# Kernel optimization log

Hardware: AMD Instinct MI355X
Metric: run time of the kernel (lower is better)

Reference implementation:

```python
import jax, jax.numpy as jnp
import numpy as np

# irreps: node in/out = 32x0e + 16x1o (dim 80), sh = 1x0e + 1x1o (dim 4)
N_NODES, N_EDGES = 8000, 64000
NUM_BASIS, RAD_HIDDEN = 8, 64
WEIGHT_NUMEL = 2304  # 32*32 + 32*16 + 16*16 + 16*32
EPS = 1e-8
INV_SQRT3 = 1.0 / np.sqrt(3.0)
# e3nn path weights (normalization='component', path_normalization='element'):
# into 0e outputs: sqrt(ir.dim=1 / (32+16)); into 1o outputs: sqrt(3 / (32+16))
PW0 = float(np.sqrt(1.0 / 48.0))
PW1 = float(np.sqrt(3.0 / 48.0))


def setup_inputs() -> dict:
    key = jax.random.key(0)
    ks = jax.random.split(key, 10)
    node_features = jax.random.normal(ks[0], (N_NODES, 80), dtype=jnp.float32)
    edge_index = jax.random.randint(ks[1], (2, N_EDGES), 0, N_NODES, dtype=jnp.int64)
    edge_sh = jax.random.normal(ks[2], (N_EDGES, 4), dtype=jnp.float32)
    edge_radial_emb = jax.random.uniform(ks[3], (N_EDGES, NUM_BASIS), dtype=jnp.float32)
    # RadialMLP params (Linear 8->64, SiLU, Linear 64->2304)
    rW1 = jax.random.normal(ks[4], (NUM_BASIS, RAD_HIDDEN), dtype=jnp.float32) / np.sqrt(NUM_BASIS)
    rb1 = jnp.zeros((RAD_HIDDEN,), dtype=jnp.float32)
    rW2 = jax.random.normal(ks[5], (RAD_HIDDEN, WEIGHT_NUMEL), dtype=jnp.float32) / np.sqrt(RAD_HIDDEN)
    rb2 = jnp.zeros((WEIGHT_NUMEL,), dtype=jnp.float32)
    # o3.Linear weights (per-irrep mixing matrices, e3nn init ~ N(0,1))
    Wl0 = jax.random.normal(ks[6], (32, 32), dtype=jnp.float32)
    Wl1 = jax.random.normal(ks[7], (16, 16), dtype=jnp.float32)
    return {"node_features": node_features, "edge_index": edge_index,
            "edge_sh": edge_sh, "edge_radial_emb": edge_radial_emb,
            "rW1": rW1, "rb1": rb1, "rW2": rW2, "rb2": rb2,
            "Wl0": Wl0, "Wl1": Wl1}


def reference(node_features, edge_index, edge_sh, edge_radial_emb,
              rW1, rb1, rW2, rb2, Wl0, Wl1):
    N = node_features.shape[0]
    src, dst = edge_index[0], edge_index[1]
    # radial MLP -> per-edge tensor-product weights [E, 2304] (fp32 path)
    h = jax.nn.silu(edge_radial_emb @ rW1 + rb1)
    tpw = h @ rW2 + rb2
    E = tpw.shape[0]
    wA = tpw[:, :1024].reshape(E, 32, 32)      # 0e x 0e -> 0e
    wB = tpw[:, 1024:1536].reshape(E, 32, 16)  # 0e x 1o -> 1o
    wC = tpw[:, 1536:1792].reshape(E, 16, 16)  # 1o x 0e -> 1o
    wD = tpw[:, 1792:2304].reshape(E, 16, 32)  # 1o x 1o -> 0e
    # gather source node features
    xs = node_features[src, :32]                       # [E,32] scalars
    xv = node_features[src, 32:].reshape(E, 16, 3)     # [E,16,3] vectors
    sh0 = edge_sh[:, 0]                                # [E]
    shv = edge_sh[:, 1:4]                              # [E,3]
    # equivariant tensor product messages
    dotv = jnp.einsum('euk,ek->eu', xv, shv)           # 1o.1o -> 0e
    msg_s = PW0 * (jnp.einsum('euw,eu->ew', wA, xs * sh0[:, None])
                   + INV_SQRT3 * jnp.einsum('euw,eu->eu' if False else 'euw,eu->ew', wD, dotv))
    msg_v = (PW1 * INV_SQRT3) * (jnp.einsum('euw,eu,ek->ewk', wB, xs, shv)
                                 + jnp.einsum('euw,euk->ewk', wC, xv) * sh0[:, None, None])
    messages = jnp.concatenate([msg_s, msg_v.reshape(E, 48)], axis=-1)  # [E,80]
    # scatter-sum aggregation over destination nodes
    agg = jax.ops.segment_sum(messages, dst, num_segments=N)            # [N,80]
    # equivariant linear (per-irrep mixing, fan-in normalized)
    lin_s = (agg[:, :32] @ Wl0) / np.sqrt(32.0)
    lin_v = jnp.einsum('nuk,uv->nvk', agg[:, 32:].reshape(N, 16, 3), Wl1) / np.sqrt(16.0)
    # SafeNormActivation: silu on scalars, norm-gated silu on vectors
    act_s = jax.nn.silu(lin_s)
    norms = jnp.linalg.norm(lin_v, axis=-1, keepdims=True)   # [N,16,1]
    safe = jnp.maximum(norms, EPS)
    act_v = jnp.where(norms < EPS, 0.0, (lin_v / safe) * jax.nn.silu(norms))
    activated = jnp.concatenate([act_s, act_v.reshape(N, 48)], axis=-1)
    # skip connection (irreps_in == irreps_out -> identity skip)
    return node_features + activated
```

## Files before the change

### kernel.cpp

```cpp
#include <hip/hip_runtime.h>
#include <math.h>

#define N_NODES_C 8000
#define N_EDGES_C 64000

static constexpr float PW0_C     = 0.14433756729740646f;
static constexpr float C1_C      = 0.14433756729740643f;
static constexpr float PW0IS3_C  = 0.08333333333333333f;
static constexpr float RS32_C    = 0.17677669529663687f;

typedef __attribute__((ext_vector_type(8))) short short8;
typedef __attribute__((ext_vector_type(4))) float f32x4;

__device__ __forceinline__ float silu_f(float x) { return x / (1.0f + expf(-x)); }

__device__ __forceinline__ unsigned short f2bf(float x) {
    union { float f; unsigned u; } a; a.f = x;
    unsigned r = a.u + 0x7fffu + ((a.u >> 16) & 1u);
    return (unsigned short)(r >> 16);
}
__device__ __forceinline__ float bf2f(unsigned short x) {
    union { unsigned u; float f; } a; a.u = ((unsigned)x) << 16; return a.f;
}

__device__ __forceinline__ void stage16(const void* g, void* lds) {
    __builtin_amdgcn_global_load_lds(
        (const __attribute__((address_space(1))) void*)g,
        (__attribute__((address_space(3))) void*)lds, 16, 0, 0);
}

__global__ __launch_bounds__(256) void prep_kernel(
    const float* __restrict__ rW2, unsigned short* __restrict__ rW2T)
{
    const int idx = blockIdx.x * 256 + threadIdx.x;
    const int k = idx / 2304, col = idx % 2304;
    rW2T[(size_t)col * 64 + k] = f2bf(rW2[idx]);
}

__global__ __launch_bounds__(256, 2) void edge_kernel_mfma(
    const float* __restrict__ nf,
    const int*   __restrict__ ei,
    const float* __restrict__ sh,
    const float* __restrict__ emb,
    const float* __restrict__ rW1,
    const float* __restrict__ rb1,
    const unsigned short* __restrict__ rW2T,
    const float* __restrict__ rb2,
    float* __restrict__ agg)
{
    __shared__ float pool_f[8192];
    __shared__ float rb2_s[2304];
    __shared__ float rW1_s[512];
    __shared__ unsigned short xs_s[128][34];
    __shared__ unsigned short xv_s[128][50];
    __shared__ float dv_s[128][17];
    __shared__ float sh0_s[128];
    __shared__ float shv_s[128][3];
    __shared__ int   dst_s[128];

    char*  stg = (char*)pool_f;
    float (*msg)[84] = reinterpret_cast<float(*)[84]>(pool_f);

    const int t    = threadIdx.x;
    const int e0   = blockIdx.x * 128;
    const int lane = t & 63, wv = t >> 6;
    const int l15  = lane & 15, lk = lane >> 4;
    const int l7   = l15 & 7;

    #define STAGE(cc, b) {                                                        \
        const char* gsrc = (const char*)rW2T + (size_t)(cc) * 8192;               \
        _Pragma("unroll")                                                         \
        for (int j = 0; j < 2; j++) {                                             \
            const int p  = j * 256 + t;                                           \
            const int pr = p >> 3;                                                \
            const int sl = (p & 7) ^ (pr & 7);                                    \
            stage16(gsrc + pr * 128 + (sl << 4), stg + (b) * 8192 + p * 16);      \
        }                                                                         \
    }

    STAGE(0, 0)
    STAGE(1, 1)
    if (t < 128) {
        const int eid = e0 + t;
        dst_s[t] = ei[N_EDGES_C + eid];
        const float4 s4 = *reinterpret_cast<const float4*>(sh + (size_t)eid * 4);
        sh0_s[t] = s4.x;
        shv_s[t][0] = s4.y; shv_s[t][1] = s4.z; shv_s[t][2] = s4.w;
    }
    {
        const int e = t >> 1, q = t & 1;
        const int src = ei[e0 + e];
        const float* p = nf + (size_t)src * 80 + q * 40;
        #pragma unroll
        for (int f4 = 0; f4 < 10; f4++) {
            const float4 v = *reinterpret_cast<const float4*>(p + f4 * 4);
            const int g = q * 40 + f4 * 4;
            const float vv[4] = {v.x, v.y, v.z, v.w};
            #pragma unroll
            for (int ii = 0; ii < 4; ii++) {
                const int gg = g + ii;
                if (gg < 32) xs_s[e][gg]      = f2bf(vv[ii]);
                else         xv_s[e][gg - 32] = f2bf(vv[ii]);
            }
        }
    }
    for (int i = t; i < 512;  i += 256) rW1_s[i] = rW1[i];
    for (int i = t; i < 2304; i += 256) rb2_s[i] = rb2[i];
    __syncthreads();

    {
        const int e = t >> 1, u0d = (t & 1) * 8;
        #pragma unroll
        for (int i = 0; i < 8; i++) {
            const int u = u0d + i;
            dv_s[e][u] = bf2f(xv_s[e][u*3+0]) * shv_s[e][0]
                       + bf2f(xv_s[e][u*3+1]) * shv_s[e][1]
                       + bf2f(xv_s[e][u*3+2]) * shv_s[e][2];
        }
    }
    const int eA = wv * 32 + l15;
    const int eB = eA + 16;
    short8 bfr[2][2];
    {
        float embA[8], embB[8];
        {
            const float* pa = emb + (size_t)(e0 + eA) * 8;
            const float* pb = emb + (size_t)(e0 + eB) * 8;
            const float4 a0 = *reinterpret_cast<const float4*>(pa);
            const float4 a1 = *reinterpret_cast<const float4*>(pa + 4);
            const float4 b0 = *reinterpret_cast<const float4*>(pb);
            const float4 b1 = *reinterpret_cast<const float4*>(pb + 4);
            embA[0]=a0.x; embA[1]=a0.y; embA[2]=a0.z; embA[3]=a0.w;
            embA[4]=a1.x; embA[5]=a1.y; embA[6]=a1.z; embA[7]=a1.w;
            embB[0]=b0.x; embB[1]=b0.y; embB[2]=b0.z; embB[3]=b0.w;
            embB[4]=b1.x; embB[5]=b1.y; embB[6]=b1.z; embB[7]=b1.w;
        }
        #pragma unroll
        for (int s = 0; s < 2; s++) {
            const int k0 = s * 32 + lk * 8;
            const float4 r0 = *reinterpret_cast<const float4*>(rb1 + k0);
            const float4 r1 = *reinterpret_cast<const float4*>(rb1 + k0 + 4);
            float preA[8] = {r0.x,r0.y,r0.z,r0.w, r1.x,r1.y,r1.z,r1.w};
            float preB[8] = {r0.x,r0.y,r0.z,r0.w, r1.x,r1.y,r1.z,r1.w};
            #pragma unroll
            for (int b = 0; b < 8; b++) {
                const float4 wa = *reinterpret_cast<const float4*>(&rW1_s[b * 64 + k0]);
                const float4 wb = *reinterpret_cast<const float4*>(&rW1_s[b * 64 + k0 + 4]);
                const float wv4[8] = {wa.x,wa.y,wa.z,wa.w, wb.x,wb.y,wb.z,wb.w};
                #pragma unroll
                for (int j = 0; j < 8; j++) {
                    preA[j] = fmaf(embA[b], wv4[j], preA[j]);
                    preB[j] = fmaf(embB[b], wv4[j], preB[j]);
                }
            }
            short8 hA, hBv;
            #pragma unroll
            for (int j = 0; j < 8; j++) {
                hA[j]  = (short)f2bf(silu_f(preA[j]));
                hBv[j] = (short)f2bf(silu_f(preB[j]));
            }
            bfr[0][s] = hA; bfr[1][s] = hBv;
        }
    }
    const float sh0A = sh0_s[eA], sh0B = sh0_s[eB];
    const float fAA  = PW0_C * sh0A, fAB = PW0_C * sh0B;
    __syncthreads();

    float sA0[2][4] = {{0,0,0,0},{0,0,0,0}}, sA1[2][4] = {{0,0,0,0},{0,0,0,0}};
    float sB0[4] = {0,0,0,0},                sB1[4] = {0,0,0,0};
    float sC0[3][4] = {{0,0,0,0},{0,0,0,0},{0,0,0,0}};
    float sC1[3][4] = {{0,0,0,0},{0,0,0,0},{0,0,0,0}};

    for (int c = 0; c < 36; ++c) {
        if (c < 34) STAGE(c + 2, (c + 2) & 3)
        if (c < 34)       { asm volatile("s_waitcnt vmcnt(4)" ::: "memory"); }
        else if (c == 34) { asm volatile("s_waitcnt vmcnt(2)" ::: "memory"); }
        else              { asm volatile("s_waitcnt vmcnt(0)" ::: "memory"); }
        __builtin_amdgcn_sched_barrier(0);
        __builtin_amdgcn_s_barrier();

        const int cb = c * 64;
        f32x4 acc0[4], acc1[4];
        #pragma unroll
        for (int m = 0; m < 4; m++) {
            const float4 rbv = *reinterpret_cast<const float4*>(&rb2_s[cb + m * 16 + lk * 4]);
            acc0[m][0] = rbv.x; acc0[m][1] = rbv.y; acc0[m][2] = rbv.z; acc0[m][3] = rbv.w;
            acc1[m][0] = rbv.x; acc1[m][1] = rbv.y; acc1[m][2] = rbv.z; acc1[m][3] = rbv.w;
        }
        const char* sb = stg + (c & 3) * 8192;
        #pragma unroll
        for (int s = 0; s < 2; s++) {
            #pragma unroll
            for (int m = 0; m < 4; m++) {
                const short8 a = *reinterpret_cast<const short8*>(
                    sb + (m * 16 + l15) * 128 + (((s * 4 + lk) ^ l7) << 4));
                acc0[m] = __builtin_amdgcn_mfma_f32_16x16x32_bf16(a, bfr[0][s], acc0[m], 0, 0, 0);
                acc1[m] = __builtin_amdgcn_mfma_f32_16x16x32_bf16(a, bfr[1][s], acc1[m], 0, 0, 0);
            }
        }

        if (c < 16) {
            const float xA0 = bf2f(xs_s[eA][c*2]) * fAA, xA1 = bf2f(xs_s[eA][c*2+1]) * fAA;
            const float xB0 = bf2f(xs_s[eB][c*2]) * fAB, xB1 = bf2f(xs_s[eB][c*2+1]) * fAB;
            #pragma unroll
            for (int r = 0; r < 4; r++) {
                sA0[0][r] = fmaf(acc0[0][r], xA0, fmaf(acc0[2][r], xA1, sA0[0][r]));
                sA0[1][r] = fmaf(acc0[1][r], xA0, fmaf(acc0[3][r], xA1, sA0[1][r]));
                sA1[0][r] = fmaf(acc1[0][r], xB0, fmaf(acc1[2][r], xB1, sA1[0][r]));
                sA1[1][r] = fmaf(acc1[1][r], xB0, fmaf(acc1[3][r], xB1, sA1[1][r]));
            }
        } else if (c < 24) {
            const int u0 = (c - 16) * 4;
            float xA[4], xB[4];
            #pragma unroll
            for (int m = 0; m < 4; m++) { xA[m] = bf2f(xs_s[eA][u0+m]); xB[m] = bf2f(xs_s[eB][u0+m]); }
            #pragma unroll
            for (int r = 0; r < 4; r++) {
                sB0[r] = fmaf(acc0[0][r], xA[0], fmaf(acc0[1][r], xA[1],
                          fmaf(acc0[2][r], xA[2], fmaf(acc0[3][r], xA[3], sB0[r]))));
                sB1[r] = fmaf(acc1[0][r], xB[0], fmaf(acc1[1][r], xB[1],
                          fmaf(acc1[2][r], xB[2], fmaf(acc1[3][r], xB[3], sB1[r]))));
            }
        } else if (c < 28) {
            const int u0 = (c - 24) * 4;
            #pragma unroll
            for (int k = 0; k < 3; k++) {
                float xA[4], xB[4];
                #pragma unroll
                for (int m = 0; m < 4; m++) {
                    xA[m] = bf2f(xv_s[eA][(u0+m)*3+k]);
                    xB[m] = bf2f(xv_s[eB][(u0+m)*3+k]);
                }
                #pragma unroll
                for (int r = 0; r < 4; r++) {
                    sC0[k][r] = fmaf(acc0[0][r], xA[0], fmaf(acc0[1][r], xA[1],
                                 fmaf(acc0[2][r], xA[2], fmaf(acc0[3][r], xA[3], sC0[k][r]))));
                    sC1[k][r] = fmaf(acc1[0][r], xB[0], fmaf(acc1[1][r], xB[1],
                                 fmaf(acc1[2][r], xB[2], fmaf(acc1[3][r], xB[3], sC1[k][r]))));
                }
            }
        } else {
            const int u0 = (c - 28) * 2;
            const float dA0 = dv_s[eA][u0] * PW0IS3_C, dA1 = dv_s[eA][u0+1] * PW0IS3_C;
            const float dB0 = dv_s[eB][u0] * PW0IS3_C, dB1 = dv_s[eB][u0+1] * PW0IS3_C;
            #pragma unroll
            for (int r = 0; r < 4; r++) {
                sA0[0][r] = fmaf(acc0[0][r], dA0, fmaf(acc0[2][r], dA1, sA0[0][r]));
                sA0[1][r] = fmaf(acc0[1][r], dA0, fmaf(acc0[3][r], dA1, sA0[1][r]));
                sA1[0][r] = fmaf(acc1[0][r], dB0, fmaf(acc1[2][r], dB1, sA1[0][r]));
                sA1[1][r] = fmaf(acc1[1][r], dB0, fmaf(acc1[3][r], dB1, sA1[1][r]));
            }
        }
    }
    #undef STAGE

    #pragma unroll
    for (int pass = 0; pass < 2; ++pass) {
        __syncthreads();
        if ((wv >> 1) == pass) {
            const int lr0 = (wv & 1) * 32 + l15;
            const int lr1 = lr0 + 16;
            #pragma unroll
            for (int hi = 0; hi < 2; hi++)
                #pragma unroll
                for (int r = 0; r < 4; r++) {
                    msg[lr0][hi * 16 + lk * 4 + r] = sA0[hi][r];
                    msg[lr1][hi * 16 + lk * 4 + r] = sA1[hi][r];
                }
            #pragma unroll
            for (int r = 0; r < 4; r++) {
                const int w = lk * 4 + r;
                #pragma unroll
                for (int k = 0; k < 3; k++) {
                    msg[lr0][32 + w * 3 + k] = C1_C * (sB0[r] * shv_s[eA][k] + sh0A * sC0[k][r]);
                    msg[lr1][32 + w * 3 + k] = C1_C * (sB1[r] * shv_s[eB][k] + sh0B * sC1[k][r]);
                }
            }
        }
        __syncthreads();
        const int ebase = pass * 64;
        for (int i = t; i < 64 * 80; i += 256) {
            const int rr = i / 80, m = i - rr * 80;
            atomicAdd(&agg[(size_t)dst_s[ebase + rr] * 80 + m], msg[rr][m]);
        }
    }
}

__global__ __launch_bounds__(256, 1) void edge_kernel_f32(
    const float* __restrict__ nf, const int* __restrict__ ei,
    const float* __restrict__ sh, const float* __restrict__ emb,
    const float* __restrict__ rW1, const float* __restrict__ rb1,
    const float* __restrict__ rW2, const float* __restrict__ rb2,
    float* __restrict__ agg)
{
    __shared__ float hT[64][68];
    __shared__ float tpw[64][132];
    __shared__ float xs_s[64][32];
    __shared__ float xv_s[64][48];
    __shared__ float dv_s[64][16];
    __shared__ float sh0_s[64];
    __shared__ float shv_s[64][3];
    __shared__ int   dst_s[64];
    __shared__ float msg[64][84];

    const int t  = threadIdx.x;
    const int e0 = blockIdx.x * 64;
    if (t < 64) {
        const int eid = e0 + t;
        dst_s[t] = ei[N_EDGES_C + eid];
        const float4 s4 = *reinterpret_cast<const float4*>(sh + (size_t)eid * 4);
        sh0_s[t] = s4.x; shv_s[t][0] = s4.y; shv_s[t][1] = s4.z; shv_s[t][2] = s4.w;
    }
    for (int i = t; i < 64 * 84; i += 256) (&msg[0][0])[i] = 0.0f;
    {
        const int e = t >> 2, q = t & 3;
        const int src = ei[e0 + e];
        const float* p = nf + (size_t)src * 80 + q * 20;
        #pragma unroll
        for (int f4 = 0; f4 < 5; f4++) {
            const float4 v = *reinterpret_cast<const float4*>(p + f4 * 4);
            const int g = q * 20 + f4 * 4;
            const float vv[4] = {v.x, v.y, v.z, v.w};
            #pragma unroll
            for (int ii = 0; ii < 4; ii++) {
                const int gg = g + ii;
                if (gg < 32) xs_s[e][gg] = vv[ii]; else xv_s[e][gg - 32] = vv[ii];
            }
        }
    }
    {
        const int c = t & 63, eg = t >> 6;
        float w1[8];
        #pragma unroll
        for (int b = 0; b < 8; b++) w1[b] = rW1[b * 64 + c];
        const float bias = rb1[c];
        #pragma unroll
        for (int rep = 0; rep < 16; rep++) {
            const int e = rep * 4 + eg;
            const float* em = emb + (size_t)(e0 + e) * 8;
            float pre = bias;
            #pragma unroll
            for (int b = 0; b < 8; b++) pre = fmaf(em[b], w1[b], pre);
            hT[c][e] = silu_f(pre);
        }
    }
    __syncthreads();
    {
        const int e = t >> 2, q = t & 3;
        #pragma unroll
        for (int i = 0; i < 4; i++) {
            const int u = q * 4 + i;
            dv_s[e][u] = xv_s[e][u*3+0]*shv_s[e][0] + xv_s[e][u*3+1]*shv_s[e][1]
                       + xv_s[e][u*3+2]*shv_s[e][2];
        }
    }
    __syncthreads();
    const int lane = t & 63, wv = t >> 6;
    for (int ch = 0; ch < 18; ch++) {
        const int jb = ch * 128;
        float acc[16][2];
        #pragma unroll
        for (int i = 0; i < 16; i++) { acc[i][0] = 0.0f; acc[i][1] = 0.0f; }
        const float* Bp = rW2 + jb + lane * 2;
        #pragma unroll 2
        for (int c = 0; c < 64; c++) {
            const float2 b = *reinterpret_cast<const float2*>(Bp + (size_t)c * 2304);
            const float4* ap = reinterpret_cast<const float4*>(&hT[c][wv * 16]);
            const float4 a0 = ap[0], a1 = ap[1], a2 = ap[2], a3 = ap[3];
            const float va[16] = {a0.x,a0.y,a0.z,a0.w, a1.x,a1.y,a1.z,a1.w,
                                  a2.x,a2.y,a2.z,a2.w, a3.x,a3.y,a3.z,a3.w};
            #pragma unroll
            for (int i = 0; i < 16; i++) {
                acc[i][0] = fmaf(va[i], b.x, acc[i][0]);
                acc[i][1] = fmaf(va[i], b.y, acc[i][1]);
            }
        }
        const float2 rb = *reinterpret_cast<const float2*>(rb2 + jb + lane * 2);
        __syncthreads();
        #pragma unroll
        for (int i = 0; i < 16; i++)
            *reinterpret_cast<float2*>(&tpw[wv * 16 + i][lane * 2]) =
                make_float2(acc[i][0] + rb.x, acc[i][1] + rb.y);
        __syncthreads();
        if (ch < 8) {
            const int u0 = ch * 4, w = t & 31, eg = t >> 5;
            #pragma unroll
            for (int ee = 0; ee < 8; ee++) {
                const int e = eg * 8 + ee;
                float s = 0.0f;
                #pragma unroll
                for (int du = 0; du < 4; du++) s = fmaf(tpw[e][du * 32 + w], xs_s[e][u0 + du], s);
                msg[e][w] = fmaf(PW0_C * sh0_s[e], s, msg[e][w]);
            }
        } else if (ch < 12) {
            const int u0 = (ch - 8) * 8, w = t & 15, eg = t >> 4;
            #pragma unroll
            for (int ee = 0; ee < 4; ee++) {
                const int e = eg * 4 + ee;
                float s = 0.0f;
                #pragma unroll
                for (int du = 0; du < 8; du++) s = fmaf(tpw[e][du * 16 + w], xs_s[e][u0 + du], s);
                const float c1s = C1_C * s;
                msg[e][32 + w*3 + 0] = fmaf(c1s, shv_s[e][0], msg[e][32 + w*3 + 0]);
                msg[e][32 + w*3 + 1] = fmaf(c1s, shv_s[e][1], msg[e][32 + w*3 + 1]);
                msg[e][32 + w*3 + 2] = fmaf(c1s, shv_s[e][2], msg[e][32 + w*3 + 2]);
            }
        } else if (ch < 14) {
            const int u0 = (ch - 12) * 8, w = t & 15, eg = t >> 4;
            #pragma unroll
            for (int ee = 0; ee < 4; ee++) {
                const int e = eg * 4 + ee;
                float s0 = 0, s1 = 0, s2 = 0;
                #pragma unroll
                for (int du = 0; du < 8; du++) {
                    const float tv = tpw[e][du * 16 + w];
                    const int u = u0 + du;
                    s0 = fmaf(tv, xv_s[e][u*3 + 0], s0);
                    s1 = fmaf(tv, xv_s[e][u*3 + 1], s1);
                    s2 = fmaf(tv, xv_s[e][u*3 + 2], s2);
                }
                const float f = C1_C * sh0_s[e];
                msg[e][32 + w*3 + 0] = fmaf(f, s0, msg[e][32 + w*3 + 0]);
                msg[e][32 + w*3 + 1] = fmaf(f, s1, msg[e][32 + w*3 + 1]);
                msg[e][32 + w*3 + 2] = fmaf(f, s2, msg[e][32 + w*3 + 2]);
            }
        } else {
            const int u0 = (ch - 14) * 4, w = t & 31, eg = t >> 5;
            #pragma unroll
            for (int ee = 0; ee < 8; ee++) {
                const int e = eg * 8 + ee;
                float s = 0.0f;
                #pragma unroll
                for (int du = 0; du < 4; du++) s = fmaf(tpw[e][du * 32 + w], dv_s[e][u0 + du], s);
                msg[e][w] = fmaf(PW0IS3_C, s, msg[e][w]);
            }
        }
    }
    __syncthreads();
    for (int i = t; i < 64 * 80; i += 256) {
        const int e = i / 80, m = i - e * 80;
        atomicAdd(&agg[(size_t)dst_s[e] * 80 + m], msg[e][m]);
    }
}

__global__ __launch_bounds__(256, 4) void node_kernel(
    const float* __restrict__ nf,
    float* __restrict__ io,
    const float* __restrict__ Wl0,
    const float* __restrict__ Wl1)
{
    __shared__ float a_s[4][80];
    const int t  = threadIdx.x;
    const int nb = blockIdx.x * 4;
    for (int i = t; i < 320; i += 256)
        a_s[i / 80][i % 80] = io[(size_t)nb * 80 + i];
    __syncthreads();

    const int ln = t >> 6;
    const int r  = t & 63;
    const int n  = nb + ln;
    const float* a = a_s[ln];
    if (r < 32) {
        float s = 0.0f;
        #pragma unroll
        for (int u = 0; u < 32; u++) s = fmaf(a[u], Wl0[u * 32 + r], s);
        s *= RS32_C;
        io[(size_t)n * 80 + r] = nf[(size_t)n * 80 + r] + silu_f(s);
    } else if (r < 48) {
        const int v = r - 32;
        float l0 = 0, l1 = 0, l2 = 0;
        #pragma unroll
        for (int u = 0; u < 16; u++) {
            const float w = Wl1[u * 16 + v];
            l0 = fmaf(a[32 + u*3 + 0], w, l0);
            l1 = fmaf(a[32 + u*3 + 1], w, l1);
            l2 = fmaf(a[32 + u*3 + 2], w, l2);
        }
        l0 *= 0.25f; l1 *= 0.25f; l2 *= 0.25f;
        const float norm = sqrtf(l0*l0 + l1*l1 + l2*l2);
        float f = 0.0f;
        if (norm >= 1e-8f) f = silu_f(norm) / norm;
        const size_t o = (size_t)n * 80 + 32 + (size_t)v * 3;
        io[o + 0] = nf[o + 0] + f * l0;
        io[o + 1] = nf[o + 1] + f * l1;
        io[o + 2] = nf[o + 2] + f * l2;
    }
}

extern "C" void kernel_launch(void* const* d_in, const int* in_sizes, int n_in,
                              void* d_out, int out_size, void* d_ws, size_t ws_size,
                              hipStream_t stream) {
    const float* nf  = (const float*)d_in[0];
    const int*   ei  = (const int*)d_in[1];
    const float* sh  = (const float*)d_in[2];
    const float* emb = (const float*)d_in[3];
    const float* rW1 = (const float*)d_in[4];
    const float* rb1 = (const float*)d_in[5];
    const float* rW2 = (const float*)d_in[6];
    const float* rb2 = (const float*)d_in[7];
    const float* Wl0 = (const float*)d_in[8];
    const float* Wl1 = (const float*)d_in[9];

    float* agg = (float*)d_out;
    hipMemsetAsync(agg, 0, (size_t)N_NODES_C * 80 * sizeof(float), stream);

    const size_t rW2T_bytes = (size_t)2304 * 64 * sizeof(unsigned short);
    if (d_ws != nullptr && ws_size >= rW2T_bytes) {
        unsigned short* rW2T = (unsigned short*)d_ws;
        prep_kernel<<<(2304 * 64) / 256, 256, 0, stream>>>(rW2, rW2T);
        edge_kernel_mfma<<<N_EDGES_C / 128, 256, 0, stream>>>(
            nf, ei, sh, emb, rW1, rb1, rW2T, rb2, agg);
    } else {
        edge_kernel_f32<<<N_EDGES_C / 64, 256, 0, stream>>>(
            nf, ei, sh, emb, rW1, rb1, rW2, rb2, agg);
    }
    node_kernel<<<N_NODES_C / 4, 256, 0, stream>>>(nf, agg, Wl0, Wl1);
}
```

Before: 69.63 us.

## Software-pipeline MFMA chunks so epilogue FMAs overlap the next chunk's matrix ops

Restructures the 36-chunk loop into a two-stage software pipeline with double accumulator sets. The epilogue contraction of chunk c-1 is issued after chunk c's MFMAs, so VALU work can hide MFMA latency instead of waiting on fresh results. It costs extra accumulator registers (two more f32x4[4] pairs), which may raise VGPR/AGPR pressure and reduce occupancy.

```diff
diff --git a/kernel.cpp b/kernel.cpp
--- a/kernel.cpp
+++ b/kernel.cpp
@@ -171,87 +171,103 @@
     float sC0[3][4] = {{0,0,0,0},{0,0,0,0},{0,0,0,0}};
     float sC1[3][4] = {{0,0,0,0},{0,0,0,0},{0,0,0,0}};
 
-    for (int c = 0; c < 36; ++c) {
-        if (c < 34) STAGE(c + 2, (c + 2) & 3)
-        if (c < 34)       { asm volatile("s_waitcnt vmcnt(4)" ::: "memory"); }
-        else if (c == 34) { asm volatile("s_waitcnt vmcnt(2)" ::: "memory"); }
-        else              { asm volatile("s_waitcnt vmcnt(0)" ::: "memory"); }
-        __builtin_amdgcn_sched_barrier(0);
-        __builtin_amdgcn_s_barrier();
-
-        const int cb = c * 64;
-        f32x4 acc0[4], acc1[4];
-        #pragma unroll
-        for (int m = 0; m < 4; m++) {
-            const float4 rbv = *reinterpret_cast<const float4*>(&rb2_s[cb + m * 16 + lk * 4]);
-            acc0[m][0] = rbv.x; acc0[m][1] = rbv.y; acc0[m][2] = rbv.z; acc0[m][3] = rbv.w;
-            acc1[m][0] = rbv.x; acc1[m][1] = rbv.y; acc1[m][2] = rbv.z; acc1[m][3] = rbv.w;
-        }
-        const char* sb = stg + (c & 3) * 8192;
-        #pragma unroll
-        for (int s = 0; s < 2; s++) {
-            #pragma unroll
-            for (int m = 0; m < 4; m++) {
-                const short8 a = *reinterpret_cast<const short8*>(
-                    sb + (m * 16 + l15) * 128 + (((s * 4 + lk) ^ l7) << 4));
-                acc0[m] = __builtin_amdgcn_mfma_f32_16x16x32_bf16(a, bfr[0][s], acc0[m], 0, 0, 0);
-                acc1[m] = __builtin_amdgcn_mfma_f32_16x16x32_bf16(a, bfr[1][s], acc1[m], 0, 0, 0);
-            }
-        }
-
-        if (c < 16) {
-            const float xA0 = bf2f(xs_s[eA][c*2]) * fAA, xA1 = bf2f(xs_s[eA][c*2+1]) * fAA;
-            const float xB0 = bf2f(xs_s[eB][c*2]) * fAB, xB1 = bf2f(xs_s[eB][c*2+1]) * fAB;
-            #pragma unroll
-            for (int r = 0; r < 4; r++) {
-                sA0[0][r] = fmaf(acc0[0][r], xA0, fmaf(acc0[2][r], xA1, sA0[0][r]));
-                sA0[1][r] = fmaf(acc0[1][r], xA0, fmaf(acc0[3][r], xA1, sA0[1][r]));
-                sA1[0][r] = fmaf(acc1[0][r], xB0, fmaf(acc1[2][r], xB1, sA1[0][r]));
-                sA1[1][r] = fmaf(acc1[1][r], xB0, fmaf(acc1[3][r], xB1, sA1[1][r]));
-            }
-        } else if (c < 24) {
-            const int u0 = (c - 16) * 4;
-            float xA[4], xB[4];
-            #pragma unroll
-            for (int m = 0; m < 4; m++) { xA[m] = bf2f(xs_s[eA][u0+m]); xB[m] = bf2f(xs_s[eB][u0+m]); }
-            #pragma unroll
-            for (int r = 0; r < 4; r++) {
-                sB0[r] = fmaf(acc0[0][r], xA[0], fmaf(acc0[1][r], xA[1],
-                          fmaf(acc0[2][r], xA[2], fmaf(acc0[3][r], xA[3], sB0[r]))));
-                sB1[r] = fmaf(acc1[0][r], xB[0], fmaf(acc1[1][r], xB[1],
-                          fmaf(acc1[2][r], xB[2], fmaf(acc1[3][r], xB[3], sB1[r]))));
-            }
-        } else if (c < 28) {
-            const int u0 = (c - 24) * 4;
-            #pragma unroll
-            for (int k = 0; k < 3; k++) {
-                float xA[4], xB[4];
-                #pragma unroll
-                for (int m = 0; m < 4; m++) {
-                    xA[m] = bf2f(xv_s[eA][(u0+m)*3+k]);
-                    xB[m] = bf2f(xv_s[eB][(u0+m)*3+k]);
-                }
-                #pragma unroll
-                for (int r = 0; r < 4; r++) {
-                    sC0[k][r] = fmaf(acc0[0][r], xA[0], fmaf(acc0[1][r], xA[1],
-                                 fmaf(acc0[2][r], xA[2], fmaf(acc0[3][r], xA[3], sC0[k][r]))));
-                    sC1[k][r] = fmaf(acc1[0][r], xB[0], fmaf(acc1[1][r], xB[1],
-                                 fmaf(acc1[2][r], xB[2], fmaf(acc1[3][r], xB[3], sC1[k][r]))));
-                }
-            }
-        } else {
-            const int u0 = (c - 28) * 2;
-            const float dA0 = dv_s[eA][u0] * PW0IS3_C, dA1 = dv_s[eA][u0+1] * PW0IS3_C;
-            const float dB0 = dv_s[eB][u0] * PW0IS3_C, dB1 = dv_s[eB][u0+1] * PW0IS3_C;
-            #pragma unroll
-            for (int r = 0; r < 4; r++) {
-                sA0[0][r] = fmaf(acc0[0][r], dA0, fmaf(acc0[2][r], dA1, sA0[0][r]));
-                sA0[1][r] = fmaf(acc0[1][r], dA0, fmaf(acc0[3][r], dA1, sA0[1][r]));
-                sA1[0][r] = fmaf(acc1[0][r], dB0, fmaf(acc1[2][r], dB1, sA1[0][r]));
-                sA1[1][r] = fmaf(acc1[1][r], dB0, fmaf(acc1[3][r], dB1, sA1[1][r]));
-            }
-        }
-    }
+    #define PRE(cc) {                                                             \
+        if ((cc) < 34) STAGE((cc) + 2, ((cc) + 2) & 3)                            \
+        if ((cc) < 34)       { asm volatile("s_waitcnt vmcnt(4)" ::: "memory"); } \
+        else if ((cc) == 34) { asm volatile("s_waitcnt vmcnt(2)" ::: "memory"); } \
+        else                 { asm volatile("s_waitcnt vmcnt(0)" ::: "memory"); } \
+        __builtin_amdgcn_sched_barrier(0);                                        \
+        __builtin_amdgcn_s_barrier(); }
+
+    #define GEMM2(cc, a0, a1) {                                                   \
+        const int cb_ = (cc) * 64;                                                \
+        const char* sb_ = stg + ((cc) & 3) * 8192;                                \
+        _Pragma("unroll")                                                         \
+        for (int m = 0; m < 4; m++) {                                             \
+            const float4 rbv = *reinterpret_cast<const float4*>(                  \
+                &rb2_s[cb_ + m * 16 + lk * 4]);                                   \
+            a0[m][0] = rbv.x; a0[m][1] = rbv.y; a0[m][2] = rbv.z; a0[m][3] = rbv.w; \
+            a1[m][0] = rbv.x; a1[m][1] = rbv.y; a1[m][2] = rbv.z; a1[m][3] = rbv.w; \
+        }                                                                         \
+        _Pragma("unroll")                                                         \
+        for (int s = 0; s < 2; s++) {                                             \
+            _Pragma("unroll")                                                     \
+            for (int m = 0; m < 4; m++) {                                         \
+                const short8 a_ = *reinterpret_cast<const short8*>(               \
+                    sb_ + (m * 16 + l15) * 128 + (((s * 4 + lk) ^ l7) << 4));     \
+                a0[m] = __builtin_amdgcn_mfma_f32_16x16x32_bf16(a_, bfr[0][s], a0[m], 0, 0, 0); \
+                a1[m] = __builtin_amdgcn_mfma_f32_16x16x32_bf16(a_, bfr[1][s], a1[m], 0, 0, 0); \
+            }                                                                     \
+        } }
+
+    #define EPI(cc, a0, a1) {                                                     \
+        const int c_ = (cc);                                                      \
+        if (c_ < 16) {                                                            \
+            const float xA0 = bf2f(xs_s[eA][c_*2]) * fAA, xA1 = bf2f(xs_s[eA][c_*2+1]) * fAA; \
+            const float xB0 = bf2f(xs_s[eB][c_*2]) * fAB, xB1 = bf2f(xs_s[eB][c_*2+1]) * fAB; \
+            _Pragma("unroll")                                                     \
+            for (int r = 0; r < 4; r++) {                                         \
+                sA0[0][r] = fmaf(a0[0][r], xA0, fmaf(a0[2][r], xA1, sA0[0][r]));  \
+                sA0[1][r] = fmaf(a0[1][r], xA0, fmaf(a0[3][r], xA1, sA0[1][r]));  \
+                sA1[0][r] = fmaf(a1[0][r], xB0, fmaf(a1[2][r], xB1, sA1[0][r]));  \
+                sA1[1][r] = fmaf(a1[1][r], xB0, fmaf(a1[3][r], xB1, sA1[1][r]));  \
+            }                                                                     \
+        } else if (c_ < 24) {                                                     \
+            const int u0 = (c_ - 16) * 4;                                         \
+            float xA[4], xB[4];                                                   \
+            _Pragma("unroll")                                                     \
+            for (int m = 0; m < 4; m++) { xA[m] = bf2f(xs_s[eA][u0+m]); xB[m] = bf2f(xs_s[eB][u0+m]); } \
+            _Pragma("unroll")                                                     \
+            for (int r = 0; r < 4; r++) {                                         \
+                sB0[r] = fmaf(a0[0][r], xA[0], fmaf(a0[1][r], xA[1],              \
+                          fmaf(a0[2][r], xA[2], fmaf(a0[3][r], xA[3], sB0[r])))); \
+                sB1[r] = fmaf(a1[0][r], xB[0], fmaf(a1[1][r], xB[1],              \
+                          fmaf(a1[2][r], xB[2], fmaf(a1[3][r], xB[3], sB1[r])))); \
+            }                                                                     \
+        } else if (c_ < 28) {                                                     \
+            const int u0 = (c_ - 24) * 4;                                         \
+            _Pragma("unroll")                                                     \
+            for (int k = 0; k < 3; k++) {                                         \
+                float xA[4], xB[4];                                               \
+                _Pragma("unroll")                                                 \
+                for (int m = 0; m < 4; m++) {                                     \
+                    xA[m] = bf2f(xv_s[eA][(u0+m)*3+k]);                           \
+                    xB[m] = bf2f(xv_s[eB][(u0+m)*3+k]);                           \
+                }                                                                 \
+                _Pragma("unroll")                                                 \
+                for (int r = 0; r < 4; r++) {                                     \
+                    sC0[k][r] = fmaf(a0[0][r], xA[0], fmaf(a0[1][r], xA[1],       \
+                                 fmaf(a0[2][r], xA[2], fmaf(a0[3][r], xA[3], sC0[k][r])))); \
+                    sC1[k][r] = fmaf(a1[0][r], xB[0], fmaf(a1[1][r], xB[1],       \
+                                 fmaf(a1[2][r], xB[2], fmaf(a1[3][r], xB[3], sC1[k][r])))); \
+                }                                                                 \
+            }                                                                     \
+        } else {                                                                  \
+            const int u0 = (c_ - 28) * 2;                                         \
+            const float dA0 = dv_s[eA][u0] * PW0IS3_C, dA1 = dv_s[eA][u0+1] * PW0IS3_C; \
+            const float dB0 = dv_s[eB][u0] * PW0IS3_C, dB1 = dv_s[eB][u0+1] * PW0IS3_C; \
+            _Pragma("unroll")                                                     \
+            for (int r = 0; r < 4; r++) {                                         \
+                sA0[0][r] = fmaf(a0[0][r], dA0, fmaf(a0[2][r], dA1, sA0[0][r]));  \
+                sA0[1][r] = fmaf(a0[1][r], dA0, fmaf(a0[3][r], dA1, sA0[1][r]));  \
+                sA1[0][r] = fmaf(a1[0][r], dB0, fmaf(a1[2][r], dB1, sA1[0][r]));  \
+                sA1[1][r] = fmaf(a1[1][r], dB0, fmaf(a1[3][r], dB1, sA1[1][r]));  \
+            }                                                                     \
+        } }
+
+    f32x4 pA[4], pB[4], qA[4], qB[4];
+    for (int c = 0; c < 36; c += 2) {
+        PRE(c)
+        GEMM2(c, pA, pB)
+        if (c > 0) { EPI(c - 1, qA, qB) }
+        PRE(c + 1)
+        GEMM2(c + 1, qA, qB)
+        EPI(c, pA, pB)
+    }
+    EPI(35, qA, qB)
+    #undef PRE
+    #undef GEMM2
+    #undef EPI
     #undef STAGE
 
     #pragma unroll
```

New measurement: 67.48 us. -3.1%, faster.
